# Kernel optimization log

Hardware: AMD Instinct MI355X
Metric: run time of the kernel (lower is better)

## Reference

```python
import jax, jax.numpy as jnp
import numpy as np

ALPHA = 0.1
NUM_CLASSES = 10000
FEAT_DIM = 256
BATCH = 8192


def setup_inputs() -> dict:
    key = jax.random.key(0)
    k1, k2, k3 = jax.random.split(key, 3)
    feat = jax.random.normal(k1, (BATCH, FEAT_DIM), dtype=jnp.float32)
    label = jax.random.randint(k2, (BATCH,), 0, NUM_CLASSES, dtype=jnp.int64)
    # centers parameter, initialized ~ randn as in the torch constructor
    centers = jax.random.normal(k3, (NUM_CLASSES, FEAT_DIM), dtype=jnp.float32)
    return {"feat": feat, "label": label, "centers": centers}


def reference(feat, label, centers):
    B = feat.shape[0]
    # dist[b,c] = ||feat[b] - centers[c]||^2, computed in GEMM form:
    # ||f||^2 + ||c||^2 - 2 f.c  (same math as the broadcast diff^2 sum)
    f_sq = jnp.sum(feat * feat, axis=-1, keepdims=True)          # [B, 1]
    c_sq = jnp.sum(centers * centers, axis=-1)[None, :]          # [1, C]
    cross = jnp.einsum('bd,cd->bc', feat, centers)               # [B, C]
    dist = f_sq + c_sq - 2.0 * cross                             # [B, C]

    # one-hot margin scaling: y_onehot = alpha * onehot(label) + 1
    onehot = jax.nn.one_hot(label, NUM_CLASSES, dtype=dist.dtype)  # [B, C]
    margin_dist = dist * (onehot * ALPHA + 1.0)

    margin_logits = -0.5 * margin_dist
    logits = -0.5 * dist

    # likelihood: mean over batch of 0.5 * ||feat - centers[label]||^2
    cdiff = feat - centers[label]                                 # [B, D]
    likelihood = jnp.sum(cdiff * cdiff) / (2.0 * B)
    return (logits, margin_logits, likelihood)
```

## Files before the change

### kernel.cpp

```cpp
#include <hip/hip_runtime.h>
#include <hip/hip_bf16.h>


#define ALPHA_ 0.1f
constexpr int BATCH = 8192;
constexpr int NCLS  = 10000;
constexpr int FDIM  = 256;

typedef __attribute__((ext_vector_type(8))) short bf16x8;
typedef __attribute__((ext_vector_type(4))) float f32x4;

__device__ __forceinline__ unsigned short f2bf(float f) {
  unsigned int u = __float_as_uint(f);
  u += 0x7FFF + ((u >> 16) & 1);
  return (unsigned short)(u >> 16);
}

__global__ void prep_kernel(const float* __restrict__ feat,
                            const float* __restrict__ centers,
                            unsigned short* __restrict__ fbf,
                            unsigned short* __restrict__ cbf,
                            float* __restrict__ fsq,
                            float* __restrict__ csq) {
  int gw = (int)((blockIdx.x * blockDim.x + threadIdx.x) >> 6);
  int lane = threadIdx.x & 63;
  if (gw >= BATCH + NCLS) return;
  const float* src; unsigned short* dst; float* sq;
  if (gw < BATCH) {
    src = feat + (size_t)gw * FDIM; dst = fbf + (size_t)gw * FDIM; sq = fsq + gw;
  } else {
    int r = gw - BATCH;
    src = centers + (size_t)r * FDIM; dst = cbf + (size_t)r * FDIM; sq = csq + r;
  }
  float4 v = reinterpret_cast<const float4*>(src)[lane];
  ushort4 b;
  b.x = f2bf(v.x); b.y = f2bf(v.y); b.z = f2bf(v.z); b.w = f2bf(v.w);
  reinterpret_cast<ushort4*>(dst)[lane] = b;
  float s = v.x*v.x + v.y*v.y + v.z*v.z + v.w*v.w;
  #pragma unroll
  for (int off = 32; off >= 1; off >>= 1) s += __shfl_xor(s, off, 64);
  if (lane == 0) *sq = s;
}

#define BM 128
#define BN 128
#define BK 64

__global__ __launch_bounds__(512, 4)
void gemm_kernel(const unsigned short* __restrict__ fbf,
                 const unsigned short* __restrict__ cbf,
                 const float* __restrict__ fsq,
                 const float* __restrict__ csq,
                 const int* __restrict__ label,
                 float* __restrict__ out_logits,
                 float* __restrict__ out_margin,
                 float* __restrict__ lik_row) {
  __shared__ unsigned short As[2][BM * BK];
  __shared__ unsigned short Bs[2][BN * BK];

  const int NTN = (NCLS + BN - 1) / BN;
  const int NWG = (BATCH / BM) * NTN;

  int bid = blockIdx.x;
  int wg = (bid & 7) * (NWG >> 3) + (bid >> 3);
  int mt = wg / NTN;
  int nt = wg - mt * NTN;

  const int tid  = threadIdx.x;
  const int lane = tid & 63;
  const int wid  = tid >> 6;
  const int wr   = (wid >> 2) * 64;
  const int wc   = (wid & 3) * 32;

  f32x4 acc[4][2];
  #pragma unroll
  for (int i = 0; i < 4; i++)
    #pragma unroll
    for (int j = 0; j < 2; j++) acc[i][j] = (f32x4){0.f, 0.f, 0.f, 0.f};

  const int sr = tid >> 3;
  const int sc = tid & 7;
  const size_t a_base = (size_t)(mt * BM) * FDIM;
  const int c0 = nt * BN;

  bf16x8 va[2], vb[2];
  #define LOADT(kc_) do {                                                      \
    int k0 = (kc_) * BK;                                                       \
    _Pragma("unroll")                                                          \
    for (int j = 0; j < 2; ++j) {                                              \
      int r = j * 64 + sr;                                                     \
      va[j] = *reinterpret_cast<const bf16x8*>(fbf + a_base + (size_t)r * FDIM + k0 + sc * 8); \
      int cc = c0 + r; cc = (cc < NCLS) ? cc : (NCLS - 1);                     \
      vb[j] = *reinterpret_cast<const bf16x8*>(cbf + (size_t)cc * FDIM + k0 + sc * 8); \
    }                                                                          \
  } while (0)
  #define STORET(b_) do {                                                      \
    _Pragma("unroll")                                                          \
    for (int j = 0; j < 2; ++j) {                                              \
      int r = j * 64 + sr;                                                     \
      int off = r * BK + ((sc ^ (r & 7)) * 8);                                 \
      *reinterpret_cast<bf16x8*>(&As[b_][off]) = va[j];                        \
      *reinterpret_cast<bf16x8*>(&Bs[b_][off]) = vb[j];                        \
    }                                                                          \
  } while (0)

  LOADT(0);
  STORET(0);

  #pragma unroll
  for (int kc = 0; kc < FDIM / BK; ++kc) {
    const int cur = kc & 1;
    if (kc < FDIM / BK - 1) LOADT(kc + 1);
    __syncthreads();
    #pragma unroll
    for (int kk = 0; kk < BK / 32; ++kk) {
      const int ch = kk * 4 + (lane >> 4);
      bf16x8 a[4], b[2];
      #pragma unroll
      for (int i = 0; i < 4; i++) {
        int row = wr + i * 16 + (lane & 15);
        a[i] = *reinterpret_cast<const bf16x8*>(&As[cur][row * BK + ((ch ^ (row & 7)) * 8)]);
      }
      #pragma unroll
      for (int j = 0; j < 2; j++) {
        int row = wc + j * 16 + (lane & 15);
        b[j] = *reinterpret_cast<const bf16x8*>(&Bs[cur][row * BK + ((ch ^ (row & 7)) * 8)]);
      }
      #pragma unroll
      for (int i = 0; i < 4; i++)
        #pragma unroll
        for (int j = 0; j < 2; j++)
          acc[i][j] = __builtin_amdgcn_mfma_f32_16x16x32_bf16(b[j], a[i], acc[i][j], 0, 0, 0);
    }
    if (kc < FDIM / BK - 1) STORET(cur ^ 1);
  }

  const int mloc = wr + (lane & 15);
  const int nbase = wc + ((lane >> 4) << 2);
  #pragma unroll
  for (int i = 0; i < 4; i++) {
    int m = mt * BM + mloc + i * 16;
    float fs = fsq[m];
    int lb = label[m];
    size_t rowoff = (size_t)m * NCLS;
    #pragma unroll
    for (int j = 0; j < 2; j++) {
      int n0 = c0 + nbase + j * 16;
      if (n0 >= NCLS) continue;
      float4 cs = *reinterpret_cast<const float4*>(&csq[n0]);
      f32x4 v = acc[i][j];
      f32x4 lg;
      lg[0] = v[0] - 0.5f * (fs + cs.x);
      lg[1] = v[1] - 0.5f * (fs + cs.y);
      lg[2] = v[2] - 0.5f * (fs + cs.z);
      lg[3] = v[3] - 0.5f * (fs + cs.w);
      *reinterpret_cast<f32x4*>(&out_logits[rowoff + n0]) = lg;
      f32x4 mg;
      mg[0] = (lb == n0    ) ? lg[0] * (1.0f + ALPHA_) : lg[0];
      mg[1] = (lb == n0 + 1) ? lg[1] * (1.0f + ALPHA_) : lg[1];
      mg[2] = (lb == n0 + 2) ? lg[2] * (1.0f + ALPHA_) : lg[2];
      mg[3] = (lb == n0 + 3) ? lg[3] * (1.0f + ALPHA_) : lg[3];
      *reinterpret_cast<f32x4*>(&out_margin[rowoff + n0]) = mg;
      if (lb == n0)          lik_row[m] = -lg[0];
      else if (lb == n0 + 1) lik_row[m] = -lg[1];
      else if (lb == n0 + 2) lik_row[m] = -lg[2];
      else if (lb == n0 + 3) lik_row[m] = -lg[3];
    }
  }
  #undef LOADT
  #undef STORET
}

__global__ void lik_reduce_kernel(const float* __restrict__ lik_row,
                                  float* __restrict__ out) {
  int t = threadIdx.x;
  float v = 0.f;
  #pragma unroll
  for (int i = 0; i < BATCH / 1024; i++) v += lik_row[t + i * 1024];
  #pragma unroll
  for (int off = 32; off >= 1; off >>= 1) v += __shfl_xor(v, off, 64);
  __shared__ float red[16];
  if ((t & 63) == 0) red[t >> 6] = v;
  __syncthreads();
  if (t == 0) {
    float s = 0.f;
    #pragma unroll
    for (int i = 0; i < 16; i++) s += red[i];
    out[0] = s * (1.0f / BATCH);
  }
}

extern "C" void kernel_launch(void* const* d_in, const int* in_sizes, int n_in,
                              void* d_out, int out_size, void* d_ws, size_t ws_size,
                              hipStream_t stream) {
  const float* feat    = (const float*)d_in[0];
  const int*   label   = (const int*)d_in[1];
  const float* centers = (const float*)d_in[2];

  float* out        = (float*)d_out;
  float* out_logits = out;
  float* out_margin = out + (size_t)BATCH * NCLS;
  float* out_lik    = out + 2 * (size_t)BATCH * NCLS;

  char* ws = (char*)d_ws;
  unsigned short* fbf = (unsigned short*)ws;
  unsigned short* cbf = (unsigned short*)(ws + (size_t)BATCH * FDIM * 2);
  float* fsq     = (float*)(ws + (size_t)BATCH * FDIM * 2 + (size_t)NCLS * FDIM * 2);
  float* csq     = fsq + BATCH;
  float* lik_row = csq + NCLS;

  prep_kernel<<<(BATCH + NCLS) / 4, 256, 0, stream>>>(feat, centers, fbf, cbf, fsq, csq);
  gemm_kernel<<<(BATCH / BM) * ((NCLS + BN - 1) / BN), 512, 0, stream>>>(
      fbf, cbf, fsq, csq, label, out_logits, out_margin, lik_row);
  lik_reduce_kernel<<<1, 1024, 0, stream>>>(lik_row, out_lik);
}
```

Baseline: 200.2 us.

## Make GEMM persistent and overlap previous tile's output stores with next tile's MFMAs

Turns the GEMM into a persistent kernel with a fixed grid of 512 workgroups that loop over output tiles. Each tile's finished logits are kept in registers and written out interleaved with the k-loop of the next tile, so the large output stores overlap with MFMA work instead of forming a serial epilogue. This adds register pressure from the second accumulator set and cuts the number of resident waves. The store ordering also changes, since one tile's writes are spread across the next tile's compute.

```diff
diff --git a/kernel.cpp b/kernel.cpp
--- a/kernel.cpp
+++ b/kernel.cpp
@@ -45,6 +45,9 @@
 #define BM 128
 #define BN 128
 #define BK 64
+#define GRID 512
+constexpr int NTN = 79;
+constexpr int NWG = (BATCH / BM) * NTN;
 
 __global__ __launch_bounds__(512, 4)
 void gemm_kernel(const unsigned short* __restrict__ fbf,
@@ -58,42 +61,34 @@
   __shared__ unsigned short As[2][BM * BK];
   __shared__ unsigned short Bs[2][BN * BK];
 
-  const int NTN = (NCLS + BN - 1) / BN;
-  const int NWG = (BATCH / BM) * NTN;
-
-  int bid = blockIdx.x;
-  int wg = (bid & 7) * (NWG >> 3) + (bid >> 3);
-  int mt = wg / NTN;
-  int nt = wg - mt * NTN;
-
+  const int bid  = blockIdx.x;
   const int tid  = threadIdx.x;
   const int lane = tid & 63;
   const int wid  = tid >> 6;
   const int wr   = (wid >> 2) * 64;
   const int wc   = (wid & 3) * 32;
+  const int sr   = tid >> 3;
+  const int sc   = tid & 7;
+  const int mloc  = wr + (lane & 15);
+  const int nbase = wc + ((lane >> 4) << 2);
 
   f32x4 acc[4][2];
-  #pragma unroll
-  for (int i = 0; i < 4; i++)
-    #pragma unroll
-    for (int j = 0; j < 2; j++) acc[i][j] = (f32x4){0.f, 0.f, 0.f, 0.f};
-
-  const int sr = tid >> 3;
-  const int sc = tid & 7;
-  const size_t a_base = (size_t)(mt * BM) * FDIM;
-  const int c0 = nt * BN;
+  f32x4 oacc[4][2];
+  int   plb[4];
+  int   pmb = 0, pc0 = 0;
 
   bf16x8 va[2], vb[2];
-  #define LOADT(kc_) do {                                                      \
-    int k0 = (kc_) * BK;                                                       \
+
+  #define LOADT(abase_, c0_, k0_) do {                                         \
     _Pragma("unroll")                                                          \
     for (int j = 0; j < 2; ++j) {                                              \
       int r = j * 64 + sr;                                                     \
-      va[j] = *reinterpret_cast<const bf16x8*>(fbf + a_base + (size_t)r * FDIM + k0 + sc * 8); \
-      int cc = c0 + r; cc = (cc < NCLS) ? cc : (NCLS - 1);                     \
-      vb[j] = *reinterpret_cast<const bf16x8*>(cbf + (size_t)cc * FDIM + k0 + sc * 8); \
+      va[j] = *reinterpret_cast<const bf16x8*>(fbf + (abase_) + (size_t)r * FDIM + (k0_) + sc * 8); \
+      int cc = (c0_) + r; cc = (cc < NCLS) ? cc : (NCLS - 1);                  \
+      vb[j] = *reinterpret_cast<const bf16x8*>(cbf + (size_t)cc * FDIM + (k0_) + sc * 8); \
     }                                                                          \
   } while (0)
+
   #define STORET(b_) do {                                                      \
     _Pragma("unroll")                                                          \
     for (int j = 0; j < 2; ++j) {                                              \
@@ -104,71 +99,101 @@
     }                                                                          \
   } while (0)
 
-  LOADT(0);
-  STORET(0);
-
-  #pragma unroll
-  for (int kc = 0; kc < FDIM / BK; ++kc) {
-    const int cur = kc & 1;
-    if (kc < FDIM / BK - 1) LOADT(kc + 1);
-    __syncthreads();
-    #pragma unroll
-    for (int kk = 0; kk < BK / 32; ++kk) {
-      const int ch = kk * 4 + (lane >> 4);
-      bf16x8 a[4], b[2];
+  #define EMIT(i_) do {                                                        \
+    int m_ = pmb + (i_) * 16;                                                  \
+    size_t rowoff_ = (size_t)m_ * NCLS;                                        \
+    int lb_ = plb[i_];                                                         \
+    _Pragma("unroll")                                                          \
+    for (int j = 0; j < 2; ++j) {                                              \
+      int n0_ = pc0 + nbase + j * 16;                                          \
+      if (n0_ < NCLS) {                                                        \
+        f32x4 lg_ = oacc[i_][j];                                               \
+        *reinterpret_cast<f32x4*>(&out_logits[rowoff_ + n0_]) = lg_;           \
+        f32x4 mg_;                                                             \
+        mg_[0] = (lb_ == n0_    ) ? lg_[0] * (1.0f + ALPHA_) : lg_[0];         \
+        mg_[1] = (lb_ == n0_ + 1) ? lg_[1] * (1.0f + ALPHA_) : lg_[1];         \
+        mg_[2] = (lb_ == n0_ + 2) ? lg_[2] * (1.0f + ALPHA_) : lg_[2];         \
+        mg_[3] = (lb_ == n0_ + 3) ? lg_[3] * (1.0f + ALPHA_) : lg_[3];         \
+        *reinterpret_cast<f32x4*>(&out_margin[rowoff_ + n0_]) = mg_;           \
+        if (lb_ >= n0_ && lb_ < n0_ + 4) {                                     \
+          float v_ = (lb_ == n0_) ? lg_[0] : (lb_ == n0_ + 1) ? lg_[1]         \
+                   : (lb_ == n0_ + 2) ? lg_[2] : lg_[3];                       \
+          lik_row[m_] = -v_;                                                   \
+        }                                                                      \
+      }                                                                        \
+    }                                                                          \
+  } while (0)
+
+  for (int t = bid; t < NWG; t += GRID) {
+    int wg = (t & 7) * (NWG / 8) + (t >> 3);
+    int mt = wg / NTN;
+    int nt = wg - mt * NTN;
+    size_t a_base = (size_t)(mt * BM) * FDIM;
+    int c0 = nt * BN;
+    const int pend = (t != bid);
+
+    #pragma unroll
+    for (int i = 0; i < 4; i++)
       #pragma unroll
-      for (int i = 0; i < 4; i++) {
-        int row = wr + i * 16 + (lane & 15);
-        a[i] = *reinterpret_cast<const bf16x8*>(&As[cur][row * BK + ((ch ^ (row & 7)) * 8)]);
+      for (int j = 0; j < 2; j++) acc[i][j] = (f32x4){0.f, 0.f, 0.f, 0.f};
+
+    LOADT(a_base, c0, 0);
+    STORET(0);
+
+    #pragma unroll
+    for (int kc = 0; kc < FDIM / BK; ++kc) {
+      const int cur = kc & 1;
+      if (kc < FDIM / BK - 1) LOADT(a_base, c0, (kc + 1) * BK);
+      __syncthreads();
+      #pragma unroll
+      for (int kk = 0; kk < BK / 32; ++kk) {
+        const int ch = kk * 4 + (lane >> 4);
+        bf16x8 a[4], b[2];
+        #pragma unroll
+        for (int i = 0; i < 4; i++) {
+          int row = wr + i * 16 + (lane & 15);
+          a[i] = *reinterpret_cast<const bf16x8*>(&As[cur][row * BK + ((ch ^ (row & 7)) * 8)]);
+        }
+        #pragma unroll
+        for (int j = 0; j < 2; j++) {
+          int row = wc + j * 16 + (lane & 15);
+          b[j] = *reinterpret_cast<const bf16x8*>(&Bs[cur][row * BK + ((ch ^ (row & 7)) * 8)]);
+        }
+        #pragma unroll
+        for (int i = 0; i < 4; i++)
+          #pragma unroll
+          for (int j = 0; j < 2; j++)
+            acc[i][j] = __builtin_amdgcn_mfma_f32_16x16x32_bf16(b[j], a[i], acc[i][j], 0, 0, 0);
       }
+      if (pend) { EMIT(kc); }
+      if (kc < FDIM / BK - 1) STORET(cur ^ 1);
+    }
+
+    #pragma unroll
+    for (int i = 0; i < 4; i++) {
+      int m = mt * BM + mloc + i * 16;
+      float fs = fsq[m];
+      plb[i] = label[m];
       #pragma unroll
       for (int j = 0; j < 2; j++) {
-        int row = wc + j * 16 + (lane & 15);
-        b[j] = *reinterpret_cast<const bf16x8*>(&Bs[cur][row * BK + ((ch ^ (row & 7)) * 8)]);
+        int n0 = c0 + nbase + j * 16;
+        int nc = (n0 <= NCLS - 4) ? n0 : (NCLS - 4);
+        float4 cs = *reinterpret_cast<const float4*>(&csq[nc]);
+        oacc[i][j][0] = acc[i][j][0] - 0.5f * (fs + cs.x);
+        oacc[i][j][1] = acc[i][j][1] - 0.5f * (fs + cs.y);
+        oacc[i][j][2] = acc[i][j][2] - 0.5f * (fs + cs.z);
+        oacc[i][j][3] = acc[i][j][3] - 0.5f * (fs + cs.w);
       }
-      #pragma unroll
-      for (int i = 0; i < 4; i++)
-        #pragma unroll
-        for (int j = 0; j < 2; j++)
-          acc[i][j] = __builtin_amdgcn_mfma_f32_16x16x32_bf16(b[j], a[i], acc[i][j], 0, 0, 0);
     }
-    if (kc < FDIM / BK - 1) STORET(cur ^ 1);
+    pmb = mt * BM + mloc;
+    pc0 = c0;
   }
 
-  const int mloc = wr + (lane & 15);
-  const int nbase = wc + ((lane >> 4) << 2);
-  #pragma unroll
-  for (int i = 0; i < 4; i++) {
-    int m = mt * BM + mloc + i * 16;
-    float fs = fsq[m];
-    int lb = label[m];
-    size_t rowoff = (size_t)m * NCLS;
-    #pragma unroll
-    for (int j = 0; j < 2; j++) {
-      int n0 = c0 + nbase + j * 16;
-      if (n0 >= NCLS) continue;
-      float4 cs = *reinterpret_cast<const float4*>(&csq[n0]);
-      f32x4 v = acc[i][j];
-      f32x4 lg;
-      lg[0] = v[0] - 0.5f * (fs + cs.x);
-      lg[1] = v[1] - 0.5f * (fs + cs.y);
-      lg[2] = v[2] - 0.5f * (fs + cs.z);
-      lg[3] = v[3] - 0.5f * (fs + cs.w);
-      *reinterpret_cast<f32x4*>(&out_logits[rowoff + n0]) = lg;
-      f32x4 mg;
-      mg[0] = (lb == n0    ) ? lg[0] * (1.0f + ALPHA_) : lg[0];
-      mg[1] = (lb == n0 + 1) ? lg[1] * (1.0f + ALPHA_) : lg[1];
-      mg[2] = (lb == n0 + 2) ? lg[2] * (1.0f + ALPHA_) : lg[2];
-      mg[3] = (lb == n0 + 3) ? lg[3] * (1.0f + ALPHA_) : lg[3];
-      *reinterpret_cast<f32x4*>(&out_margin[rowoff + n0]) = mg;
-      if (lb == n0)          lik_row[m] = -lg[0];
-      else if (lb == n0 + 1) lik_row[m] = -lg[1];
-      else if (lb == n0 + 2) lik_row[m] = -lg[2];
-      else if (lb == n0 + 3) lik_row[m] = -lg[3];
-    }
-  }
+  EMIT(0); EMIT(1); EMIT(2); EMIT(3);
+
   #undef LOADT
   #undef STORET
+  #undef EMIT
 }
 
 __global__ void lik_reduce_kernel(const float* __restrict__ lik_row,
@@ -210,7 +235,7 @@
   float* lik_row = csq + NCLS;
 
   prep_kernel<<<(BATCH + NCLS) / 4, 256, 0, stream>>>(feat, centers, fbf, cbf, fsq, csq);
-  gemm_kernel<<<(BATCH / BM) * ((NCLS + BN - 1) / BN), 512, 0, stream>>>(
+  gemm_kernel<<<GRID, 512, 0, stream>>>(
       fbf, cbf, fsq, csq, label, out_logits, out_margin, lik_row);
   lik_reduce_kernel<<<1, 1024, 0, stream>>>(lik_row, out_lik);
 }
```

Result: slower. 210.4 us (+5.1%).

## Make GEMM persistent: each block loops over ten N-tiles of one M-tile

Applied to the files above, without the earlier changes.

Launches a fixed grid of 512 blocks. Each block owns one 128-row M-tile and iterates over up to ten N-tiles, instead of launching one block per output tile. The block-index mapping groups M-tiles per XCD-like group. The goal is to cut block launch overhead and reuse the A-tile through cache. In exchange, the load/compute pipeline is not overlapped across tiles, each tile adds an extra barrier, and the last sub-range per M-tile does only nine tiles, leaving some imbalance.

```diff
diff --git a/kernel.cpp b/kernel.cpp
--- a/kernel.cpp
+++ b/kernel.cpp
@@ -45,6 +45,8 @@
 #define BM 128
 #define BN 128
 #define BK 64
+#define GRID 512
+constexpr int NTN = 79;
 
 __global__ __launch_bounds__(512, 4)
 void gemm_kernel(const unsigned short* __restrict__ fbf,
@@ -58,42 +60,39 @@
   __shared__ unsigned short As[2][BM * BK];
   __shared__ unsigned short Bs[2][BN * BK];
 
-  const int NTN = (NCLS + BN - 1) / BN;
-  const int NWG = (BATCH / BM) * NTN;
-
-  int bid = blockIdx.x;
-  int wg = (bid & 7) * (NWG >> 3) + (bid >> 3);
-  int mt = wg / NTN;
-  int nt = wg - mt * NTN;
+  const int bid  = blockIdx.x;
+  const int g    = bid & 7;
+  const int s    = bid >> 3;
+  const int mt   = g * 8 + (s >> 3);
+  const int sub  = s & 7;
+  const int nt0  = sub * 10;
+  const int nt1  = (nt0 + 10 < NTN) ? (nt0 + 10) : NTN;
 
   const int tid  = threadIdx.x;
   const int lane = tid & 63;
   const int wid  = tid >> 6;
   const int wr   = (wid >> 2) * 64;
   const int wc   = (wid & 3) * 32;
+  const int sr   = tid >> 3;
+  const int sc   = tid & 7;
+  const int mloc  = wr + (lane & 15);
+  const int nbase = wc + ((lane >> 4) << 2);
+
+  const size_t a_base = (size_t)(mt * BM) * FDIM;
 
   f32x4 acc[4][2];
-  #pragma unroll
-  for (int i = 0; i < 4; i++)
-    #pragma unroll
-    for (int j = 0; j < 2; j++) acc[i][j] = (f32x4){0.f, 0.f, 0.f, 0.f};
-
-  const int sr = tid >> 3;
-  const int sc = tid & 7;
-  const size_t a_base = (size_t)(mt * BM) * FDIM;
-  const int c0 = nt * BN;
-
   bf16x8 va[2], vb[2];
-  #define LOADT(kc_) do {                                                      \
-    int k0 = (kc_) * BK;                                                       \
+
+  #define LOADT(c0_, k0_) do {                                                 \
     _Pragma("unroll")                                                          \
     for (int j = 0; j < 2; ++j) {                                              \
       int r = j * 64 + sr;                                                     \
-      va[j] = *reinterpret_cast<const bf16x8*>(fbf + a_base + (size_t)r * FDIM + k0 + sc * 8); \
-      int cc = c0 + r; cc = (cc < NCLS) ? cc : (NCLS - 1);                     \
-      vb[j] = *reinterpret_cast<const bf16x8*>(cbf + (size_t)cc * FDIM + k0 + sc * 8); \
+      va[j] = *reinterpret_cast<const bf16x8*>(fbf + a_base + (size_t)r * FDIM + (k0_) + sc * 8); \
+      int cc = (c0_) + r; cc = (cc < NCLS) ? cc : (NCLS - 1);                  \
+      vb[j] = *reinterpret_cast<const bf16x8*>(cbf + (size_t)cc * FDIM + (k0_) + sc * 8); \
     }                                                                          \
   } while (0)
+
   #define STORET(b_) do {                                                      \
     _Pragma("unroll")                                                          \
     for (int j = 0; j < 2; ++j) {                                              \
@@ -104,67 +103,76 @@
     }                                                                          \
   } while (0)
 
-  LOADT(0);
-  STORET(0);
-
-  #pragma unroll
-  for (int kc = 0; kc < FDIM / BK; ++kc) {
-    const int cur = kc & 1;
-    if (kc < FDIM / BK - 1) LOADT(kc + 1);
-    __syncthreads();
-    #pragma unroll
-    for (int kk = 0; kk < BK / 32; ++kk) {
-      const int ch = kk * 4 + (lane >> 4);
-      bf16x8 a[4], b[2];
+  for (int nt = nt0; nt < nt1; ++nt) {
+    const int c0 = nt * BN;
+
+    #pragma unroll
+    for (int i = 0; i < 4; i++)
       #pragma unroll
-      for (int i = 0; i < 4; i++) {
-        int row = wr + i * 16 + (lane & 15);
-        a[i] = *reinterpret_cast<const bf16x8*>(&As[cur][row * BK + ((ch ^ (row & 7)) * 8)]);
+      for (int j = 0; j < 2; j++) acc[i][j] = (f32x4){0.f, 0.f, 0.f, 0.f};
+
+    LOADT(c0, 0);
+    STORET(0);
+
+    #pragma unroll
+    for (int kc = 0; kc < FDIM / BK; ++kc) {
+      const int cur = kc & 1;
+      if (kc < FDIM / BK - 1) LOADT(c0, (kc + 1) * BK);
+      __syncthreads();
+      #pragma unroll
+      for (int kk = 0; kk < BK / 32; ++kk) {
+        const int ch = kk * 4 + (lane >> 4);
+        bf16x8 a[4], b[2];
+        #pragma unroll
+        for (int i = 0; i < 4; i++) {
+          int row = wr + i * 16 + (lane & 15);
+          a[i] = *reinterpret_cast<const bf16x8*>(&As[cur][row * BK + ((ch ^ (row & 7)) * 8)]);
+        }
+        #pragma unroll
+        for (int j = 0; j < 2; j++) {
+          int row = wc + j * 16 + (lane & 15);
+          b[j] = *reinterpret_cast<const bf16x8*>(&Bs[cur][row * BK + ((ch ^ (row & 7)) * 8)]);
+        }
+        #pragma unroll
+        for (int i = 0; i < 4; i++)
+          #pragma unroll
+          for (int j = 0; j < 2; j++)
+            acc[i][j] = __builtin_amdgcn_mfma_f32_16x16x32_bf16(b[j], a[i], acc[i][j], 0, 0, 0);
       }
+      if (kc < FDIM / BK - 1) STORET(cur ^ 1);
+      else __syncthreads();
+    }
+
+    #pragma unroll
+    for (int i = 0; i < 4; i++) {
+      int m = mt * BM + mloc + i * 16;
+      float fs = fsq[m];
+      int lb = label[m];
+      size_t rowoff = (size_t)m * NCLS;
       #pragma unroll
       for (int j = 0; j < 2; j++) {
-        int row = wc + j * 16 + (lane & 15);
-        b[j] = *reinterpret_cast<const bf16x8*>(&Bs[cur][row * BK + ((ch ^ (row & 7)) * 8)]);
+        int n0 = c0 + nbase + j * 16;
+        if (n0 >= NCLS) continue;
+        float4 cs = *reinterpret_cast<const float4*>(&csq[n0]);
+        f32x4 v = acc[i][j];
+        f32x4 lg;
+        lg[0] = v[0] - 0.5f * (fs + cs.x);
+        lg[1] = v[1] - 0.5f * (fs + cs.y);
+        lg[2] = v[2] - 0.5f * (fs + cs.z);
+        lg[3] = v[3] - 0.5f * (fs + cs.w);
+        *reinterpret_cast<f32x4*>(&out_logits[rowoff + n0]) = lg;
+        f32x4 mg;
+        mg[0] = (lb == n0    ) ? lg[0] * (1.0f + ALPHA_) : lg[0];
+        mg[1] = (lb == n0 + 1) ? lg[1] * (1.0f + ALPHA_) : lg[1];
+        mg[2] = (lb == n0 + 2) ? lg[2] * (1.0f + ALPHA_) : lg[2];
+        mg[3] = (lb == n0 + 3) ? lg[3] * (1.0f + ALPHA_) : lg[3];
+        *reinterpret_cast<f32x4*>(&out_margin[rowoff + n0]) = mg;
+        if (lb >= n0 && lb < n0 + 4) {
+          float lv = (lb == n0) ? lg[0] : (lb == n0 + 1) ? lg[1]
+                   : (lb == n0 + 2) ? lg[2] : lg[3];
+          lik_row[m] = -lv;
+        }
       }
-      #pragma unroll
-      for (int i = 0; i < 4; i++)
-        #pragma unroll
-        for (int j = 0; j < 2; j++)
-          acc[i][j] = __builtin_amdgcn_mfma_f32_16x16x32_bf16(b[j], a[i], acc[i][j], 0, 0, 0);
-    }
-    if (kc < FDIM / BK - 1) STORET(cur ^ 1);
-  }
-
-  const int mloc = wr + (lane & 15);
-  const int nbase = wc + ((lane >> 4) << 2);
-  #pragma unroll
-  for (int i = 0; i < 4; i++) {
-    int m = mt * BM + mloc + i * 16;
-    float fs = fsq[m];
-    int lb = label[m];
-    size_t rowoff = (size_t)m * NCLS;
-    #pragma unroll
-    for (int j = 0; j < 2; j++) {
-      int n0 = c0 + nbase + j * 16;
-      if (n0 >= NCLS) continue;
-      float4 cs = *reinterpret_cast<const float4*>(&csq[n0]);
-      f32x4 v = acc[i][j];
-      f32x4 lg;
-      lg[0] = v[0] - 0.5f * (fs + cs.x);
-      lg[1] = v[1] - 0.5f * (fs + cs.y);
-      lg[2] = v[2] - 0.5f * (fs + cs.z);
-      lg[3] = v[3] - 0.5f * (fs + cs.w);
-      *reinterpret_cast<f32x4*>(&out_logits[rowoff + n0]) = lg;
-      f32x4 mg;
-      mg[0] = (lb == n0    ) ? lg[0] * (1.0f + ALPHA_) : lg[0];
-      mg[1] = (lb == n0 + 1) ? lg[1] * (1.0f + ALPHA_) : lg[1];
-      mg[2] = (lb == n0 + 2) ? lg[2] * (1.0f + ALPHA_) : lg[2];
-      mg[3] = (lb == n0 + 3) ? lg[3] * (1.0f + ALPHA_) : lg[3];
-      *reinterpret_cast<f32x4*>(&out_margin[rowoff + n0]) = mg;
-      if (lb == n0)          lik_row[m] = -lg[0];
-      else if (lb == n0 + 1) lik_row[m] = -lg[1];
-      else if (lb == n0 + 2) lik_row[m] = -lg[2];
-      else if (lb == n0 + 3) lik_row[m] = -lg[3];
     }
   }
   #undef LOADT
@@ -210,7 +218,7 @@
   float* lik_row = csq + NCLS;
 
   prep_kernel<<<(BATCH + NCLS) / 4, 256, 0, stream>>>(feat, centers, fbf, cbf, fsq, csq);
-  gemm_kernel<<<(BATCH / BM) * ((NCLS + BN - 1) / BN), 512, 0, stream>>>(
+  gemm_kernel<<<GRID, 512, 0, stream>>>(
       fbf, cbf, fsq, csq, label, out_logits, out_margin, lik_row);
   lik_reduce_kernel<<<1, 1024, 0, stream>>>(lik_row, out_lik);
 }
```

Measured after the change: 269.7 us. +34.8%, slower.
